# Kernel tuning notes

Hardware: AMD Instinct MI355X
Metric: run time of the kernel (lower is better)

## Reference

```python
import jax, jax.numpy as jnp
import numpy as np

B, N, C = 4, 2048, 1024
H = 16
D = C // H  # head_dim = 64
EPS = 1e-5


def layer_norm(x, g, b):
    mu = jnp.mean(x, axis=-1, keepdims=True)
    var = jnp.var(x, axis=-1, keepdims=True)
    return (x - mu) * jax.lax.rsqrt(var + EPS) * g + b


def setup_inputs() -> dict:
    key = jax.random.key(0)
    ks = jax.random.split(key, 12)
    s = 0.02
    return {
        "x": jax.random.normal(ks[0], (B, N, C), dtype=jnp.float32),
        "Wqkv": jax.random.normal(ks[1], (C, 3 * C), dtype=jnp.float32) * s,
        "bqkv": jnp.zeros((3 * C,), dtype=jnp.float32),
        "Wproj": jax.random.normal(ks[2], (C, C), dtype=jnp.float32) * s,
        "bproj": jnp.zeros((C,), dtype=jnp.float32),
        "g1": jnp.ones((C,), dtype=jnp.float32),
        "b1": jnp.zeros((C,), dtype=jnp.float32),
        "g2": jnp.ones((C,), dtype=jnp.float32),
        "b2": jnp.zeros((C,), dtype=jnp.float32),
        "W1": jax.random.normal(ks[3], (C, 4 * C), dtype=jnp.float32) * s,
        "bf1": jnp.zeros((4 * C,), dtype=jnp.float32),
        "W2": jax.random.normal(ks[4], (4 * C, C), dtype=jnp.float32) * s,
        "bf2": jnp.zeros((C,), dtype=jnp.float32),
    }


def reference(x, Wqkv, bqkv, Wproj, bproj, g1, b1, g2, b2, W1, bf1, W2, bf2):
    # Pre-norm MHA (dropout = identity in eval mode)
    shortcut = x
    h = layer_norm(x, g1, b1)
    qkv = h @ Wqkv + bqkv                       # [B,N,3C]
    qkv = qkv.reshape(B, N, 3, H, D)
    q = jnp.transpose(qkv[:, :, 0], (0, 2, 1, 3))  # [B,H,N,D]
    k = jnp.transpose(qkv[:, :, 1], (0, 2, 1, 3))
    v = jnp.transpose(qkv[:, :, 2], (0, 2, 1, 3))
    scale = D ** -0.5
    attn = jnp.einsum("bhqd,bhkd->bhqk", q, k) * scale
    attn = jax.nn.softmax(attn, axis=-1)
    o = jnp.einsum("bhqk,bhkd->bhqd", attn, v)  # [B,H,N,D]
    o = jnp.transpose(o, (0, 2, 1, 3)).reshape(B, N, C)
    x = o @ Wproj + bproj + shortcut
    # FFN with exact GELU (torch nn.GELU default)
    h2 = layer_norm(x, g2, b2)
    ffn = jax.nn.gelu(h2 @ W1 + bf1, approximate=False) @ W2 + bf2
    return x + ffn
```

## Files before the change

kernel.cpp:

```cpp
#include <hip/hip_runtime.h>
#include <math.h>

using u16 = unsigned short;
typedef __bf16 bf16x8 __attribute__((ext_vector_type(8)));
typedef float f32x4 __attribute__((ext_vector_type(4)));
typedef short s16x4 __attribute__((ext_vector_type(4)));

__device__ __forceinline__ float b2f(u16 u) {
    union { unsigned u; float f; } c; c.u = ((unsigned)u) << 16; return c.f;
}
__device__ __forceinline__ u16 f2b(float f) {
    union { float f; unsigned u; } c; c.f = f;
    return (u16)((c.u + 0x7fffu + ((c.u >> 16) & 1u)) >> 16);
}
__device__ __forceinline__ u16 chop(float f) {
    union { float f; unsigned u; } c; c.f = f;
    return (u16)(c.u >> 16);
}

struct F8 { float v[8]; };
__device__ __forceinline__ F8 unpack8(uint4 r) {
    F8 o;
    o.v[0] = b2f((u16)r.x); o.v[1] = b2f((u16)(r.x >> 16));
    o.v[2] = b2f((u16)r.y); o.v[3] = b2f((u16)(r.y >> 16));
    o.v[4] = b2f((u16)r.z); o.v[5] = b2f((u16)(r.z >> 16));
    o.v[6] = b2f((u16)r.w); o.v[7] = b2f((u16)(r.w >> 16));
    return o;
}

__device__ __forceinline__ void gll16(const void* g, void* l) {
    __builtin_amdgcn_global_load_lds((const __attribute__((address_space(1))) void*)g,
                                     (__attribute__((address_space(3))) void*)l, 16, 0, 0);
}

__global__ void detect_k(const u16* __restrict__ g1, int* __restrict__ flag) {
    if (threadIdx.x == 0)
        *flag = (g1[0] == 0x3F80 && g1[1] == 0x3F80) ? 0 : 1;
}

__global__ __launch_bounds__(256)
void conv_vec(const void* __restrict__ src, u16* __restrict__ dst, int n,
              const int* __restrict__ flagp) {
    const int flag = *flagp;
    const int i = blockIdx.x * 256 + threadIdx.x;
    if (i < n)
        dst[i] = flag ? f2b(((const float*)src)[i]) : ((const u16*)src)[i];
}

__global__ __launch_bounds__(256)
void transpose_k(const void* __restrict__ src, u16* __restrict__ dst,
                 int R, int Cc, int srcStride, int srcOff, const int* __restrict__ flagp) {
    const int flag = *flagp;
    __shared__ u16 t[32][33];
    const int bx = blockIdx.x * 32;
    const int by = blockIdx.y * 32;
    const int tx = threadIdx.x & 31;
    const int ty = threadIdx.x >> 5;
    if (flag) {
        const float* s = (const float*)src + srcOff;
#pragma unroll
        for (int i = 0; i < 32; i += 8)
            t[ty + i][tx] = f2b(s[(size_t)(by + ty + i) * srcStride + bx + tx]);
    } else {
        const u16* s = (const u16*)src + srcOff;
#pragma unroll
        for (int i = 0; i < 32; i += 8)
            t[ty + i][tx] = s[(size_t)(by + ty + i) * srcStride + bx + tx];
    }
    __syncthreads();
#pragma unroll
    for (int i = 0; i < 32; i += 8)
        dst[(size_t)(bx + ty + i) * R + by + tx] = t[tx][ty + i];
}

__global__ __launch_bounds__(256)
void ln_kernel(const void* __restrict__ x, const u16* __restrict__ g,
               const u16* __restrict__ b, u16* __restrict__ out,
               int srcExt, const int* __restrict__ flagp) {
    const int eff = srcExt ? *flagp : 0;
    const int row = blockIdx.x;
    const int tid = threadIdx.x;
    float v0, v1, v2, v3;
    if (eff) {
        const float4 f = *(const float4*)((const float*)x + (size_t)row * 1024 + tid * 4);
        v0 = f.x; v1 = f.y; v2 = f.z; v3 = f.w;
    } else {
        const uint2 raw = *(const uint2*)((const u16*)x + (size_t)row * 1024 + tid * 4);
        v0 = b2f((u16)raw.x); v1 = b2f((u16)(raw.x >> 16));
        v2 = b2f((u16)raw.y); v3 = b2f((u16)(raw.y >> 16));
    }
    float s  = v0 + v1 + v2 + v3;
    float ss = v0 * v0 + v1 * v1 + v2 * v2 + v3 * v3;
#pragma unroll
    for (int off = 32; off > 0; off >>= 1) {
        s  += __shfl_down(s,  off, 64);
        ss += __shfl_down(ss, off, 64);
    }
    __shared__ float red[8];
    const int wave = tid >> 6, lane = tid & 63;
    if (lane == 0) { red[wave] = s; red[4 + wave] = ss; }
    __syncthreads();
    s  = red[0] + red[1] + red[2] + red[3];
    ss = red[4] + red[5] + red[6] + red[7];
    const float mu  = s * (1.f / 1024.f);
    const float var = ss * (1.f / 1024.f) - mu * mu;
    const float rs  = rsqrtf(var + 1e-5f);
    const int c = tid * 4;
    const uint2 graw = *(const uint2*)(g + c);
    const uint2 braw = *(const uint2*)(b + c);
    u16 o0 = f2b((v0 - mu) * rs * b2f((u16)graw.x)         + b2f((u16)braw.x));
    u16 o1 = f2b((v1 - mu) * rs * b2f((u16)(graw.x >> 16)) + b2f((u16)(braw.x >> 16)));
    u16 o2 = f2b((v2 - mu) * rs * b2f((u16)graw.y)         + b2f((u16)braw.y));
    u16 o3 = f2b((v3 - mu) * rs * b2f((u16)(graw.y >> 16)) + b2f((u16)(braw.y >> 16)));
    uint2 w; w.x = (unsigned)o0 | ((unsigned)o1 << 16); w.y = (unsigned)o2 | ((unsigned)o3 << 16);
    *(uint2*)(out + (size_t)row * 1024 + c) = w;
}

template<int ACT, bool ACCUM, bool RES_EXT>
__global__ __launch_bounds__(256)
void gemm_bt(const u16* __restrict__ A, const u16* __restrict__ Bt,
             const u16* __restrict__ bias, const void* __restrict__ res,
             u16* __restrict__ C, int M, int K, int ldc, const int* __restrict__ flagp) {
    const int flag = RES_EXT ? *flagp : 0;
    __shared__ u16 As[128 * 32];
    __shared__ u16 Bs[128 * 32];
    const int tid  = threadIdx.x;
    const int lane = tid & 63;
    const int wave = tid >> 6;
    const int wr   = (wave >> 1) * 64;
    const int wc   = (wave & 1) * 64;
    const int lr   = lane & 15;
    const int quad = lane >> 4;
    const int bm = blockIdx.x * 128;
    const int bn = blockIdx.y * 128;
    const int scol = (tid & 3) * 8;
    const int srow = tid >> 2;

    f32x4 acc[4][4] = {};

    const u16* Arow0 = A  + (size_t)(bm + srow) * K + scol;
    const u16* Arow1 = A  + (size_t)(bm + 64 + srow) * K + scol;
    const u16* Brow0 = Bt + (size_t)(bn + srow) * K + scol;
    const u16* Brow1 = Bt + (size_t)(bn + 64 + srow) * K + scol;

    u16* asd0 = &As[wave * 512];
    u16* asd1 = &As[2048 + wave * 512];
    u16* bsd0 = &Bs[wave * 512];
    u16* bsd1 = &Bs[2048 + wave * 512];

    for (int k0 = 0; k0 < K; k0 += 32) {
        gll16(Arow0 + k0, asd0);
        gll16(Arow1 + k0, asd1);
        gll16(Brow0 + k0, bsd0);
        gll16(Brow1 + k0, bsd1);
        __syncthreads();
        bf16x8 af[4], bfr[4];
#pragma unroll
        for (int i = 0; i < 4; ++i)
            af[i] = *(const bf16x8*)(&As[(wr + i * 16 + lr) * 32 + quad * 8]);
#pragma unroll
        for (int j = 0; j < 4; ++j)
            bfr[j] = *(const bf16x8*)(&Bs[(wc + j * 16 + lr) * 32 + quad * 8]);
#pragma unroll
        for (int i = 0; i < 4; ++i)
#pragma unroll
            for (int j = 0; j < 4; ++j)
                acc[i][j] = __builtin_amdgcn_mfma_f32_16x16x32_bf16(af[i], bfr[j], acc[i][j], 0, 0, 0);
        __syncthreads();
    }

#pragma unroll
    for (int i = 0; i < 4; ++i) {
#pragma unroll
        for (int j = 0; j < 4; ++j) {
#pragma unroll
            for (int r = 0; r < 4; ++r) {
                const int row = bm + wr + i * 16 + quad * 4 + r;
                const int col = bn + wc + j * 16 + lr;
                const size_t idx = (size_t)row * ldc + col;
                float v = acc[i][j][r];
                if (bias) v += b2f(bias[col]);
                if (ACT == 1) v = 0.5f * v * (1.0f + erff(v * 0.70710678118654752f));
                if (res) {
                    if (RES_EXT && flag) v += ((const float*)res)[idx];
                    else                 v += b2f(((const u16*)res)[idx]);
                }
                if (ACCUM) v += b2f(C[idx]);
                C[idx] = f2b(v);
            }
        }
    }
}

__global__ __launch_bounds__(256)
void flash_attn(const u16* __restrict__ qkv, u16* __restrict__ o) {
    const int qt = blockIdx.x, bh = blockIdx.y;
    const int b = bh >> 4, h = bh & 15;
    const int qbase = qt * 128;

    __shared__ u16 smem[18432];

    const int tid  = threadIdx.x;
    const int lane = tid & 63;
    const int wave = tid >> 6;
    const int lr   = lane & 15;
    const int quad = lane >> 4;
    const int wq   = wave * 32;

    const u16* base = qkv + (size_t)b * 2048 * 3072 + h * 64;

    const int kst  = tid & 63;
    const int dseg = tid >> 6;
    const u16* ksrc0 = base + 1024 + (size_t)kst * 3072 + dseg * 16;
    const u16* vsrc0 = base + 2048 + (size_t)kst * 3072 + dseg * 16;

    {
        const int row = tid & 127, seg = tid >> 7;
        const u16* src = base + (size_t)(qbase + row) * 3072 + seg * 32;
        const int sw = (row >> 2) & 3;
        u16* dstrow = &smem[9216 + row * 64];
#pragma unroll
        for (int j = 0; j < 4; ++j) {
            F8 f = unpack8(*(const uint4*)(src + j * 8));
            u16 t[8];
#pragma unroll
            for (int e = 0; e < 8; ++e) t[e] = f2b(f.v[e] * 0.18033688011112042f);
            uint4 w;
            w.x = (unsigned)t[0] | ((unsigned)t[1] << 16);
            w.y = (unsigned)t[2] | ((unsigned)t[3] << 16);
            w.z = (unsigned)t[4] | ((unsigned)t[5] << 16);
            w.w = (unsigned)t[6] | ((unsigned)t[7] << 16);
            const int grp = seg * 2 + (j >> 1);
            *(uint4*)(dstrow + ((grp ^ sw) * 16 + (j & 1) * 8)) = w;
        }
        uint4 k0 = *(const uint4*)(ksrc0);
        uint4 k1 = *(const uint4*)(ksrc0 + 8);
        uint4 v0 = *(const uint4*)(vsrc0);
        uint4 v1 = *(const uint4*)(vsrc0 + 8);
        *(uint4*)(&smem[kst * 72 + dseg * 16])     = k0;
        *(uint4*)(&smem[kst * 72 + dseg * 16 + 8]) = k1;
        u16 vv[16];
        *(uint4*)(vv) = v0; *(uint4*)(vv + 8) = v1;
#pragma unroll
        for (int j = 0; j < 16; ++j)
            smem[4608 + (dseg * 16 + j) * 72 + kst] = vv[j];
    }
    __syncthreads();

    bf16x8 qf[2][2];
#pragma unroll
    for (int mi = 0; mi < 2; ++mi)
#pragma unroll
        for (int ks = 0; ks < 2; ++ks) {
            const int row = wq + mi * 16 + lr;
            const int phys = (ks * 2 + (quad >> 1)) ^ ((lr >> 2) & 3);
            qf[mi][ks] = *(const bf16x8*)(&smem[9216 + row * 64 + phys * 16 + (quad & 1) * 8]);
        }
    __syncthreads();

    f32x4 OT[2][4] = {};
    float lp[2] = { 0.f, 0.f };

    for (int kt = 0; kt < 32; ++kt) {
        const int cb = (kt & 1) * 9216;
        const int nb = 9216 - cb;
        uint4 nk0, nk1, nv0, nv1;
        if (kt < 31) {
            const size_t off = (size_t)(kt + 1) * 64 * 3072;
            nk0 = *(const uint4*)(ksrc0 + off);
            nk1 = *(const uint4*)(ksrc0 + off + 8);
            nv0 = *(const uint4*)(vsrc0 + off);
            nv1 = *(const uint4*)(vsrc0 + off + 8);
        }

        bf16x8 kf[4][2];
#pragma unroll
        for (int t = 0; t < 4; ++t)
#pragma unroll
            for (int ks = 0; ks < 2; ++ks)
                kf[t][ks] = *(const bf16x8*)(&smem[cb + (t * 16 + lr) * 72 + ks * 32 + quad * 8]);
        f32x4 st[4][2];
#pragma unroll
        for (int t = 0; t < 4; ++t)
#pragma unroll
            for (int mi = 0; mi < 2; ++mi) {
                f32x4 z = { 0.f, 0.f, 0.f, 0.f };
                z = __builtin_amdgcn_mfma_f32_16x16x32_bf16(kf[t][0], qf[mi][0], z, 0, 0, 0);
                st[t][mi] = __builtin_amdgcn_mfma_f32_16x16x32_bf16(kf[t][1], qf[mi][1], z, 0, 0, 0);
            }

        s16x4 pf[4][2];
#pragma unroll
        for (int t = 0; t < 4; ++t)
#pragma unroll
            for (int mi = 0; mi < 2; ++mi) {
                const float e0 = exp2f(st[t][mi][0]);
                const float e1 = exp2f(st[t][mi][1]);
                const float e2 = exp2f(st[t][mi][2]);
                const float e3 = exp2f(st[t][mi][3]);
                lp[mi] += (e0 + e1) + (e2 + e3);
                s16x4 p;
                p[0] = (short)chop(e0); p[1] = (short)chop(e1);
                p[2] = (short)chop(e2); p[3] = (short)chop(e3);
                pf[t][mi] = p;
            }

#pragma unroll
        for (int dj = 0; dj < 4; ++dj)
#pragma unroll
            for (int t = 0; t < 4; ++t) {
                const s16x4 vf = *(const s16x4*)(&smem[cb + 4608 + (dj * 16 + lr) * 72 + t * 16 + quad * 4]);
                OT[0][dj] = __builtin_amdgcn_mfma_f32_16x16x16bf16_1k(vf, pf[t][0], OT[0][dj], 0, 0, 0);
                OT[1][dj] = __builtin_amdgcn_mfma_f32_16x16x16bf16_1k(vf, pf[t][1], OT[1][dj], 0, 0, 0);
            }

        if (kt < 31) {
            *(uint4*)(&smem[nb + kst * 72 + dseg * 16])     = nk0;
            *(uint4*)(&smem[nb + kst * 72 + dseg * 16 + 8]) = nk1;
            u16 vv[16];
            *(uint4*)(vv) = nv0; *(uint4*)(vv + 8) = nv1;
#pragma unroll
            for (int j = 0; j < 16; ++j)
                smem[nb + 4608 + (dseg * 16 + j) * 72 + kst] = vv[j];
        }
        __syncthreads();
    }

#pragma unroll
    for (int mi = 0; mi < 2; ++mi) {
        float l = lp[mi];
        l += __shfl_xor(l, 16);
        l += __shfl_xor(l, 32);
        lp[mi] = 1.f / l;
    }
#pragma unroll
    for (int mi = 0; mi < 2; ++mi) {
        const float inv = lp[mi];
        const int row = qbase + wq + mi * 16 + lr;
        u16* orow = o + (size_t)(b * 2048 + row) * 1024 + h * 64;
#pragma unroll
        for (int dj = 0; dj < 4; ++dj) {
            const u16 a0 = f2b(OT[mi][dj][0] * inv);
            const u16 a1 = f2b(OT[mi][dj][1] * inv);
            const u16 a2 = f2b(OT[mi][dj][2] * inv);
            const u16 a3 = f2b(OT[mi][dj][3] * inv);
            uint2 w;
            w.x = (unsigned)a0 | ((unsigned)a1 << 16);
            w.y = (unsigned)a2 | ((unsigned)a3 << 16);
            *(uint2*)(orow + dj * 16 + quad * 4) = w;
        }
    }
}

__global__ __launch_bounds__(256)
void store_out(const u16* __restrict__ src, void* __restrict__ dst, int n,
               const int* __restrict__ flagp) {
    const int flag = *flagp;
    const int base = (blockIdx.x * 256 + threadIdx.x) * 8;
    if (base >= n) return;
    const uint4 r = *(const uint4*)(src + base);
    if (flag) {
        F8 f = unpack8(r);
        float4* d = (float4*)((float*)dst + base);
        d[0] = make_float4(f.v[0], f.v[1], f.v[2], f.v[3]);
        d[1] = make_float4(f.v[4], f.v[5], f.v[6], f.v[7]);
    } else {
        *(uint4*)((u16*)dst + base) = r;
    }
}

extern "C" void kernel_launch(void* const* d_in, const int* in_sizes, int n_in,
                              void* d_out, int out_size, void* d_ws, size_t ws_size,
                              hipStream_t stream) {
    const void* x     = d_in[0];
    const void* Wqkv  = d_in[1];
    const void* bqkv  = d_in[2];
    const void* Wproj = d_in[3];
    const void* bproj = d_in[4];
    const void* g1    = d_in[5];
    const void* b1    = d_in[6];
    const void* g2    = d_in[7];
    const void* b2    = d_in[8];
    const void* W1    = d_in[9];
    const void* bf1   = d_in[10];
    const void* W2    = d_in[11];
    const void* bf2   = d_in[12];

    char* ws = (char*)d_ws;
    int* flagp = (int*)ws;
    u16* vec  = (u16*)(ws + 256);
    u16* vbqkv = vec,        *vbproj = vec + 3072;
    u16* vg1 = vec + 4096,   *vb1 = vec + 5120;
    u16* vg2 = vec + 6144,   *vb2 = vec + 7168;
    u16* vbf1 = vec + 8192,  *vbf2 = vec + 12288;
    u16* lno = (u16*)d_out;

    detect_k<<<1, 64, 0, stream>>>((const u16*)g1, flagp);
    conv_vec<<<12, 256, 0, stream>>>(bqkv,  vbqkv, 3072, flagp);
    conv_vec<<<4,  256, 0, stream>>>(bproj, vbproj, 1024, flagp);
    conv_vec<<<4,  256, 0, stream>>>(g1, vg1, 1024, flagp);
    conv_vec<<<4,  256, 0, stream>>>(b1, vb1, 1024, flagp);
    conv_vec<<<4,  256, 0, stream>>>(g2, vg2, 1024, flagp);
    conv_vec<<<4,  256, 0, stream>>>(b2, vb2, 1024, flagp);
    conv_vec<<<16, 256, 0, stream>>>(bf1, vbf1, 4096, flagp);
    conv_vec<<<4,  256, 0, stream>>>(bf2, vbf2, 1024, flagp);

    if (ws_size >= 127000000ull) {
        u16* wT   = (u16*)(ws + 65536);
        u16* QKV  = (u16*)(ws + 9437184);
        u16* x2   = QKV;
        u16* h2   = (u16*)(ws + 26214400);
        u16* OUT2 = (u16*)(ws + 42991616);
        u16* F1   = (u16*)(ws + 59768832);
        u16* ACC  = F1;

        ln_kernel<<<8192, 256, 0, stream>>>(x, vg1, vb1, lno, 1, flagp);
        transpose_k<<<dim3(96, 32), 256, 0, stream>>>(Wqkv, wT, 1024, 3072, 3072, 0, flagp);
        gemm_bt<0, false, false><<<dim3(64, 24), 256, 0, stream>>>(
            lno, wT, vbqkv, nullptr, QKV, 8192, 1024, 3072, flagp);
        flash_attn<<<dim3(16, 64), 256, 0, stream>>>(QKV, ACC);
        transpose_k<<<dim3(32, 32), 256, 0, stream>>>(Wproj, wT, 1024, 1024, 1024, 0, flagp);
        gemm_bt<0, false, true><<<dim3(64, 8), 256, 0, stream>>>(
            ACC, wT, vbproj, x, x2, 8192, 1024, 1024, flagp);
        ln_kernel<<<8192, 256, 0, stream>>>(x2, vg2, vb2, h2, 0, flagp);
        transpose_k<<<dim3(128, 32), 256, 0, stream>>>(W1, wT, 1024, 4096, 4096, 0, flagp);
        gemm_bt<1, false, false><<<dim3(64, 32), 256, 0, stream>>>(
            h2, wT, vbf1, nullptr, F1, 8192, 1024, 4096, flagp);
        transpose_k<<<dim3(32, 128), 256, 0, stream>>>(W2, wT, 4096, 1024, 1024, 0, flagp);
        gemm_bt<0, false, false><<<dim3(64, 8), 256, 0, stream>>>(
            F1, wT, vbf2, x2, OUT2, 8192, 4096, 1024, flagp);
        store_out<<<4096, 256, 0, stream>>>(OUT2, d_out, 8388608, flagp);
    } else {
        u16* wT  = (u16*)(ws + 65536);
        u16* BIG = (u16*)(ws + 4194304);
        u16* x2  = BIG;
        u16* h2  = (u16*)(ws + 4194304 + 16777216);
        u16* f1c = (u16*)(ws + 4194304 + 33554432);
        u16* ACC = (u16*)(ws + 54525952);

        ln_kernel<<<8192, 256, 0, stream>>>(x, vg1, vb1, lno, 1, flagp);
        for (int s = 0; s < 3; ++s) {
            transpose_k<<<dim3(32, 32), 256, 0, stream>>>(Wqkv, wT, 1024, 1024, 3072, s * 1024, flagp);
            gemm_bt<0, false, false><<<dim3(64, 8), 256, 0, stream>>>(
                lno, wT, vbqkv + s * 1024, nullptr, BIG + s * 1024, 8192, 1024, 3072, flagp);
        }
        flash_attn<<<dim3(16, 64), 256, 0, stream>>>(BIG, ACC);
        transpose_k<<<dim3(32, 32), 256, 0, stream>>>(Wproj, wT, 1024, 1024, 1024, 0, flagp);
        gemm_bt<0, false, true><<<dim3(64, 8), 256, 0, stream>>>(
            ACC, wT, vbproj, x, x2, 8192, 1024, 1024, flagp);
        ln_kernel<<<8192, 256, 0, stream>>>(x2, vg2, vb2, h2, 0, flagp);
        for (int c = 0; c < 4; ++c) {
            transpose_k<<<dim3(32, 32), 256, 0, stream>>>(W1, wT, 1024, 1024, 4096, c * 1024, flagp);
            gemm_bt<1, false, false><<<dim3(64, 8), 256, 0, stream>>>(
                h2, wT, vbf1 + c * 1024, nullptr, f1c, 8192, 1024, 1024, flagp);
            transpose_k<<<dim3(32, 32), 256, 0, stream>>>(W2, wT, 1024, 1024, 1024, c * 1024 * 1024, flagp);
            if (c == 0)
                gemm_bt<0, false, false><<<dim3(64, 8), 256, 0, stream>>>(
                    f1c, wT, vbf2, nullptr, ACC, 8192, 1024, 1024, flagp);
            else if (c < 3)
                gemm_bt<0, true, false><<<dim3(64, 8), 256, 0, stream>>>(
                    f1c, wT, nullptr, nullptr, ACC, 8192, 1024, 1024, flagp);
            else
                gemm_bt<0, true, false><<<dim3(64, 8), 256, 0, stream>>>(
                    f1c, wT, nullptr, x2, ACC, 8192, 1024, 1024, flagp);
        }
        store_out<<<4096, 256, 0, stream>>>(ACC, d_out, 8388608, flagp);
    }
}
```

Before: 733.9 us.

## Add 256x256-tile GEMM with 8-wave pipelined LDS staging for large-workspace path

Adds a new GEMM kernel using 256x256 output tiles, 512 threads (8 waves), 128KB dynamic LDS with double-buffered, swizzled async global-to-LDS loads staged in quarter-tile steps, s_setprio around MFMA bursts, and an XCD-aware block-index swizzle. It replaces the four 128-tile gemm_bt calls on the large-workspace path. The aim is more data reuse per tile and better overlap of loads with MFMA. In exchange, grids become small (128 blocks for the N=1024 GEMMs), which may underfill the GPU, and register pressure rises.

```diff
diff --git a/kernel.cpp b/kernel.cpp
--- a/kernel.cpp
+++ b/kernel.cpp
@@ -192,6 +192,185 @@
     }
 }
 
+__device__ __forceinline__ void stage_half256(const u16* __restrict__ A,
+        const u16* __restrict__ Bt, char* lds, int bm, int bn, int K,
+        int H, int tid) {
+    const int t   = H >> 2;
+    const int ty  = H & 3;
+    const int k0  = t << 6;
+    const int bufo = (t & 1) << 16;
+    const u16* src;
+    int rowbase, base;
+    if (ty < 2) { src = A;  rowbase = bm + ty * 128;       base = bufo + ty * 16384; }
+    else        { src = Bt; rowbase = bn + (ty - 2) * 128; base = bufo + 32768 + (ty - 2) * 16384; }
+#pragma unroll
+    for (int i = 0; i < 2; ++i) {
+        const int w    = tid * 16 + i * 8192;
+        const int row  = w >> 7;
+        const int colB = (w & 127) ^ ((row & 7) << 4);
+        const u16* g = src + (size_t)(rowbase + row) * K + k0 + (colB >> 1);
+        char* d = lds + base + ((tid >> 6) << 10) + i * 8192;
+        gll16(g, d);
+    }
+}
+
+template<int ACT, bool RES_EXT>
+__global__ __launch_bounds__(512, 2)
+void gemm256(const u16* __restrict__ A, const u16* __restrict__ Bt,
+             const u16* __restrict__ bias, const void* __restrict__ res,
+             u16* __restrict__ C, int nbx, int K, int ldc,
+             const int* __restrict__ flagp) {
+    extern __shared__ char lds[];
+    const int flag = RES_EXT ? *flagp : 0;
+
+    const int nwg = gridDim.x;
+    const int q8  = nwg >> 3;
+    const int bid = blockIdx.x;
+    const int swz = (bid & 7) * q8 + (bid >> 3);
+    const int bm  = (swz % nbx) * 256;
+    const int bn  = (swz / nbx) * 256;
+
+    const int tid  = threadIdx.x;
+    const int lane = tid & 63, wave = tid >> 6;
+    const int lr   = lane & 15, quad = lane >> 4;
+    const int wm   = wave >> 2, wn = wave & 3;
+
+    const int nt    = K >> 6;
+    const int niter = nt >> 1;
+    const int Hmax  = nt << 2;
+
+#pragma unroll
+    for (int H = 0; H < 7; ++H)
+        stage_half256(A, Bt, lds, bm, bn, K, H, tid);
+    asm volatile("s_waitcnt vmcnt(6)" ::: "memory");
+    __builtin_amdgcn_s_barrier();
+
+    f32x4 acc[8][4] = {};
+
+    const int cq = quad * 16;
+
+    for (int it = 0; it < niter; ++it) {
+        const int  Hb     = (it << 3) + 6;
+        const bool lastit = (it == niter - 1);
+#pragma unroll
+        for (int hf = 0; hf < 2; ++hf) {
+            const int bufo = hf << 16;
+            const int Hs   = Hb + (hf << 2);
+            bf16x8 a0[4][2], a1[4][2], b0[2][2], b1[2][2];
+
+#pragma unroll
+            for (int m = 0; m < 4; ++m) {
+                const int rA = wm * 64 + m * 16 + lr;
+                const int sw = (rA & 7) << 4;
+#pragma unroll
+                for (int ks = 0; ks < 2; ++ks)
+                    a0[m][ks] = *(const bf16x8*)(lds + bufo + rA * 128 + ((ks * 64 + cq) ^ sw));
+            }
+#pragma unroll
+            for (int n = 0; n < 2; ++n) {
+                const int rB = wn * 32 + n * 16 + lr;
+                const int sw = (rB & 7) << 4;
+#pragma unroll
+                for (int ks = 0; ks < 2; ++ks)
+                    b0[n][ks] = *(const bf16x8*)(lds + bufo + 32768 + rB * 128 + ((ks * 64 + cq) ^ sw));
+            }
+            if (Hs + 1 < Hmax) stage_half256(A, Bt, lds, bm, bn, K, Hs + 1, tid);
+            __builtin_amdgcn_s_barrier();
+            asm volatile("s_waitcnt lgkmcnt(0)" ::: "memory");
+            __builtin_amdgcn_s_setprio(1);
+#pragma unroll
+            for (int m = 0; m < 4; ++m)
+#pragma unroll
+                for (int n = 0; n < 2; ++n) {
+                    acc[m][n] = __builtin_amdgcn_mfma_f32_16x16x32_bf16(a0[m][0], b0[n][0], acc[m][n], 0, 0, 0);
+                    acc[m][n] = __builtin_amdgcn_mfma_f32_16x16x32_bf16(a0[m][1], b0[n][1], acc[m][n], 0, 0, 0);
+                }
+            __builtin_amdgcn_s_setprio(0);
+            __builtin_amdgcn_s_barrier();
+
+#pragma unroll
+            for (int m = 0; m < 4; ++m) {
+                const int rA = wm * 64 + m * 16 + lr;
+                const int sw = (rA & 7) << 4;
+#pragma unroll
+                for (int ks = 0; ks < 2; ++ks)
+                    a1[m][ks] = *(const bf16x8*)(lds + bufo + 16384 + rA * 128 + ((ks * 64 + cq) ^ sw));
+            }
+            if (Hs + 2 < Hmax) stage_half256(A, Bt, lds, bm, bn, K, Hs + 2, tid);
+            __builtin_amdgcn_s_barrier();
+            asm volatile("s_waitcnt lgkmcnt(0)" ::: "memory");
+            __builtin_amdgcn_s_setprio(1);
+#pragma unroll
+            for (int m = 0; m < 4; ++m)
+#pragma unroll
+                for (int n = 0; n < 2; ++n) {
+                    acc[4 + m][n] = __builtin_amdgcn_mfma_f32_16x16x32_bf16(a1[m][0], b0[n][0], acc[4 + m][n], 0, 0, 0);
+                    acc[4 + m][n] = __builtin_amdgcn_mfma_f32_16x16x32_bf16(a1[m][1], b0[n][1], acc[4 + m][n], 0, 0, 0);
+                }
+            __builtin_amdgcn_s_setprio(0);
+            __builtin_amdgcn_s_barrier();
+
+#pragma unroll
+            for (int n = 0; n < 2; ++n) {
+                const int rB = wn * 32 + n * 16 + lr;
+                const int sw = (rB & 7) << 4;
+#pragma unroll
+                for (int ks = 0; ks < 2; ++ks)
+                    b1[n][ks] = *(const bf16x8*)(lds + bufo + 49152 + rB * 128 + ((ks * 64 + cq) ^ sw));
+            }
+            if (Hs + 3 < Hmax) stage_half256(A, Bt, lds, bm, bn, K, Hs + 3, tid);
+            __builtin_amdgcn_s_barrier();
+            asm volatile("s_waitcnt lgkmcnt(0)" ::: "memory");
+            __builtin_amdgcn_s_setprio(1);
+#pragma unroll
+            for (int m = 0; m < 4; ++m)
+#pragma unroll
+                for (int n = 0; n < 2; ++n) {
+                    acc[m][2 + n] = __builtin_amdgcn_mfma_f32_16x16x32_bf16(a0[m][0], b1[n][0], acc[m][2 + n], 0, 0, 0);
+                    acc[m][2 + n] = __builtin_amdgcn_mfma_f32_16x16x32_bf16(a0[m][1], b1[n][1], acc[m][2 + n], 0, 0, 0);
+                }
+            __builtin_amdgcn_s_setprio(0);
+            __builtin_amdgcn_s_barrier();
+
+            if (Hs + 4 < Hmax) stage_half256(A, Bt, lds, bm, bn, K, Hs + 4, tid);
+            if (lastit) asm volatile("s_waitcnt vmcnt(0)" ::: "memory");
+            else        asm volatile("s_waitcnt vmcnt(6)" ::: "memory");
+            __builtin_amdgcn_s_barrier();
+            __builtin_amdgcn_s_setprio(1);
+#pragma unroll
+            for (int m = 0; m < 4; ++m)
+#pragma unroll
+                for (int n = 0; n < 2; ++n) {
+                    acc[4 + m][2 + n] = __builtin_amdgcn_mfma_f32_16x16x32_bf16(a1[m][0], b1[n][0], acc[4 + m][2 + n], 0, 0, 0);
+                    acc[4 + m][2 + n] = __builtin_amdgcn_mfma_f32_16x16x32_bf16(a1[m][1], b1[n][1], acc[4 + m][2 + n], 0, 0, 0);
+                }
+            __builtin_amdgcn_s_setprio(0);
+            __builtin_amdgcn_s_barrier();
+        }
+    }
+
+#pragma unroll
+    for (int mi = 0; mi < 8; ++mi) {
+        const int row = bm + (mi >> 2) * 128 + wm * 64 + (mi & 3) * 16 + quad * 4;
+#pragma unroll
+        for (int nj = 0; nj < 4; ++nj) {
+            const int col = bn + (nj >> 1) * 128 + wn * 32 + (nj & 1) * 16 + lr;
+            const float bia = bias ? b2f(bias[col]) : 0.f;
+#pragma unroll
+            for (int r = 0; r < 4; ++r) {
+                const size_t idx = (size_t)(row + r) * ldc + col;
+                float v = acc[mi][nj][r] + bia;
+                if (ACT == 1) v = 0.5f * v * (1.0f + erff(v * 0.70710678118654752f));
+                if (res) {
+                    if (RES_EXT && flag) v += ((const float*)res)[idx];
+                    else                 v += b2f(((const u16*)res)[idx]);
+                }
+                C[idx] = f2b(v);
+            }
+        }
+    }
+}
+
 __global__ __launch_bounds__(256)
 void flash_attn(const u16* __restrict__ qkv, u16* __restrict__ o) {
     const int qt = blockIdx.x, bh = blockIdx.y;
@@ -395,6 +574,17 @@
     u16* vbf1 = vec + 8192,  *vbf2 = vec + 12288;
     u16* lno = (u16*)d_out;
 
+    static bool ldsInit = false;
+    if (!ldsInit) {
+        hipFuncSetAttribute((const void*)gemm256<0, false>,
+                            hipFuncAttributeMaxDynamicSharedMemorySize, 131072);
+        hipFuncSetAttribute((const void*)gemm256<0, true>,
+                            hipFuncAttributeMaxDynamicSharedMemorySize, 131072);
+        hipFuncSetAttribute((const void*)gemm256<1, false>,
+                            hipFuncAttributeMaxDynamicSharedMemorySize, 131072);
+        ldsInit = true;
+    }
+
     detect_k<<<1, 64, 0, stream>>>((const u16*)g1, flagp);
     conv_vec<<<12, 256, 0, stream>>>(bqkv,  vbqkv, 3072, flagp);
     conv_vec<<<4,  256, 0, stream>>>(bproj, vbproj, 1024, flagp);
@@ -416,19 +606,19 @@
 
         ln_kernel<<<8192, 256, 0, stream>>>(x, vg1, vb1, lno, 1, flagp);
         transpose_k<<<dim3(96, 32), 256, 0, stream>>>(Wqkv, wT, 1024, 3072, 3072, 0, flagp);
-        gemm_bt<0, false, false><<<dim3(64, 24), 256, 0, stream>>>(
-            lno, wT, vbqkv, nullptr, QKV, 8192, 1024, 3072, flagp);
+        gemm256<0, false><<<dim3(32 * 12), 512, 131072, stream>>>(
+            lno, wT, vbqkv, nullptr, QKV, 32, 1024, 3072, flagp);
         flash_attn<<<dim3(16, 64), 256, 0, stream>>>(QKV, ACC);
         transpose_k<<<dim3(32, 32), 256, 0, stream>>>(Wproj, wT, 1024, 1024, 1024, 0, flagp);
-        gemm_bt<0, false, true><<<dim3(64, 8), 256, 0, stream>>>(
-            ACC, wT, vbproj, x, x2, 8192, 1024, 1024, flagp);
+        gemm256<0, true><<<dim3(32 * 4), 512, 131072, stream>>>(
+            ACC, wT, vbproj, x, x2, 32, 1024, 1024, flagp);
         ln_kernel<<<8192, 256, 0, stream>>>(x2, vg2, vb2, h2, 0, flagp);
         transpose_k<<<dim3(128, 32), 256, 0, stream>>>(W1, wT, 1024, 4096, 4096, 0, flagp);
-        gemm_bt<1, false, false><<<dim3(64, 32), 256, 0, stream>>>(
-            h2, wT, vbf1, nullptr, F1, 8192, 1024, 4096, flagp);
+        gemm256<1, false><<<dim3(32 * 16), 512, 131072, stream>>>(
+            h2, wT, vbf1, nullptr, F1, 32, 1024, 4096, flagp);
         transpose_k<<<dim3(32, 128), 256, 0, stream>>>(W2, wT, 4096, 1024, 1024, 0, flagp);
-        gemm_bt<0, false, false><<<dim3(64, 8), 256, 0, stream>>>(
-            F1, wT, vbf2, x2, OUT2, 8192, 4096, 1024, flagp);
+        gemm256<0, false><<<dim3(32 * 4), 512, 131072, stream>>>(
+            F1, wT, vbf2, x2, OUT2, 32, 4096, 1024, flagp);
         store_out<<<4096, 256, 0, stream>>>(OUT2, d_out, 8388608, flagp);
     } else {
         u16* wT  = (u16*)(ws + 65536);
```

Result: no change. 743.6 us (+1.3%).
